# Performance work log

Hardware: AMD Instinct MI355X
Metric: run time of the kernel (lower is better)

The kernel has to match this reference:

```python
import jax, jax.numpy as jnp
import numpy as np

B, N, D = 8, 4096, 1024
S, K = 4, 16            # n_slices, per-slice codebook size (2^(16/4))
d = D // S              # slice_dim = 256
BETA = 0.25


def setup_inputs() -> dict:
    key = jax.random.key(0)
    k1, k2 = jax.random.split(key)
    h = jax.random.normal(k1, (B, N, D), dtype=jnp.float32)
    # nn.init.uniform_(codebook.weight, -1/K, 1/K)
    codebooks = jax.random.uniform(k2, (S, K, d), dtype=jnp.float32,
                                   minval=-1.0 / K, maxval=1.0 / K)
    return {"h": h, "codebooks": codebooks}


def reference(h, codebooks):
    Bb, Nn, Dd = h.shape
    Ss, Kk, dd = codebooks.shape
    sg = jax.lax.stop_gradient

    # sliced DVQ: view h as [B,N,S,d]
    ze = h.reshape(Bb, Nn, Ss, dd)

    # pairwise squared distances per slice: [B,N,S,K]
    dist = ((ze ** 2).sum(-1, keepdims=True)
            + (codebooks ** 2).sum(-1)[None, None, :, :]
            - 2.0 * jnp.einsum('bnsd,skd->bnsk', ze, codebooks))
    ids = jnp.argmin(dist, axis=-1)                         # [B,N,S] int

    # gather nearest codes: [B,N,S,d]
    zq = codebooks[jnp.arange(Ss)[None, None, :], ids]

    # per-slice VQ losses (mse over that slice), summed over slices
    loss_cb = jnp.mean((zq - sg(ze)) ** 2, axis=(0, 1, 3))  # [S]
    loss_cm = jnp.mean((ze - sg(zq)) ** 2, axis=(0, 1, 3))  # [S]
    vq_total = (loss_cb + BETA * loss_cm).sum()

    # straight-through estimator, concat slices back to [B,N,D]
    z = (ze + sg(zq - ze)).reshape(Bb, Nn, Dd)

    # pack ids: offsets are [1, K, K^2, K^3] since all slice sizes equal
    offsets = (Kk ** jnp.arange(Ss)).astype(jnp.int32)
    ids_packed = (ids.astype(jnp.int32) * offsets).sum(-1)  # [B,N]

    return (z, ids_packed, vq_total)
```

## Files before the change

kernel.cpp:

```cpp
#include <hip/hip_runtime.h>


#define D_FULL 1024
#define SEG 4
#define DSEG 256
#define KC 16

#define GLOBAL_AS __attribute__((address_space(1)))
#define LDS_AS __attribute__((address_space(3)))

static __device__ __forceinline__ void load_lds16(const void* g, void* l) {
    __builtin_amdgcn_global_load_lds((GLOBAL_AS const unsigned int*)g,
                                     (LDS_AS unsigned int*)l, 16, 0, 0);
}

__global__ __launch_bounds__(256) void dvq_prep(const float* __restrict__ cb,
                                                double* __restrict__ c2d,
                                                float* __restrict__ ids_out,
                                                float* __restrict__ loss_out) {
    __shared__ double ws[4];
    const int b = blockIdx.x;
    const int t = threadIdx.x;
    const int lane = t & 63;
    const int w = t >> 6;

    ids_out[b * 512 + t] = 0.0f;
    ids_out[b * 512 + 256 + t] = 0.0f;
    if (b == 0 && t == 0) *loss_out = 0.0f;

    double v = (double)cb[b * 256 + t];
    double sq = v * v;
#pragma unroll
    for (int off = 32; off > 0; off >>= 1)
        sq += __shfl_down(sq, off, 64);
    if (lane == 0) ws[w] = sq;
    __syncthreads();
    if (t == 0) c2d[b] = ws[0] + ws[1] + ws[2] + ws[3];
}

__global__ __launch_bounds__(512, 4) void dvq_main(const float* __restrict__ h,
                                                   const float* __restrict__ cb,
                                                   const double* __restrict__ c2d,
                                                   float* __restrict__ z_out,
                                                   float* __restrict__ ids_out,
                                                   float* __restrict__ loss_out) {
    __shared__ __align__(16) float4 hl[64 * 64];
    __shared__ __align__(16) float cbl[KC * DSEG];

    const int i = threadIdx.x;
    const int lane = i & 63;
    const int w = i >> 6;
    const int ch = __builtin_amdgcn_readfirstlane(w);

    const int s = blockIdx.x & 3;
    const long tok_base = (long)(blockIdx.x >> 2) * 64;

    char* hl_b = (char*)hl;
    char* cbl_b = (char*)cbl;

#pragma unroll
    for (int rr = 0; rr < 8; ++rr) {
        const int r = ch * 8 + rr;
        load_lds16(h + (tok_base + r) * D_FULL + (long)s * DSEG +
                       ((lane ^ r) << 2),
                   hl_b + r * 1024);
    }
#pragma unroll
    for (int half = 0; half < 2; ++half) {
        load_lds16(cb + s * (KC * DSEG) + ch * 512 + half * 256 + lane * 4,
                   cbl_b + ch * 2048 + half * 1024);
    }

    __syncthreads();

    const float* cbs = cbl + ch * 32;
    const int tk = lane;

    double dot[KC];
#pragma unroll
    for (int k = 0; k < KC; ++k) dot[k] = 0.0;
    double ze2 = 0.0;

#pragma unroll
    for (int j = 0; j < 8; ++j) {
        const int jj = ch * 8 + j;
        float4 z4 = hl[tk * 64 + (jj ^ tk)];
        double z0 = (double)z4.x, z1 = (double)z4.y;
        double z2 = (double)z4.z, z3 = (double)z4.w;
        ze2 = fma(z0, z0, ze2);
        ze2 = fma(z1, z1, ze2);
        ze2 = fma(z2, z2, ze2);
        ze2 = fma(z3, z3, ze2);
#pragma unroll
        for (int k = 0; k < KC; ++k) {
            float4 c4 = *(const float4*)(cbs + k * DSEG + j * 4);
            double a = dot[k];
            a = fma(z0, (double)c4.x, a);
            a = fma(z1, (double)c4.y, a);
            a = fma(z2, (double)c4.z, a);
            a = fma(z3, (double)c4.w, a);
            dot[k] = a;
        }
    }

    __syncthreads();
    double* part = (double*)hl;
    int* ids_l = (int*)((char*)hl + 60928);
    if (w != 0) {
        double* p = part + ((w - 1) * 64 + lane) * (KC + 1);
#pragma unroll
        for (int k = 0; k < KC; ++k) p[k] = dot[k];
        p[KC] = ze2;
    }
    __syncthreads();

    if (w == 0) {
#pragma unroll
        for (int c = 0; c < 7; ++c) {
            const double* p = part + (c * 64 + lane) * (KC + 1);
#pragma unroll
            for (int k = 0; k < KC; ++k) dot[k] += p[k];
            ze2 += p[KC];
        }

        const double* c2s = c2d + s * KC;
        double best = c2s[0] - 2.0 * dot[0];
        int bk = 0;
#pragma unroll
        for (int k = 1; k < KC; ++k) {
            double sc = c2s[k] - 2.0 * dot[k];
            if (sc < best) { best = sc; bk = k; }
        }
        ids_l[lane] = bk;

        atomicAdd(&ids_out[tok_base + lane], (float)(bk << (4 * s)));

        double mind = ze2 + best;
#pragma unroll
        for (int off = 32; off > 0; off >>= 1)
            mind += __shfl_down(mind, off, 64);
        if (lane == 0)
            atomicAdd(loss_out, (float)(mind * (1.25 / 8388608.0)));
    }
    __syncthreads();

    const float4* cbl4 = (const float4*)cbl;
#pragma unroll
    for (int r0 = 0; r0 < 8; ++r0) {
        int r = ch * 8 + r0;
        int k = ids_l[r];
        float4 v = cbl4[k * 64 + lane];
        ((float4*)(z_out + (tok_base + r) * D_FULL + (long)s * DSEG))[lane] = v;
    }
}

extern "C" void kernel_launch(void* const* d_in, const int* in_sizes, int n_in,
                              void* d_out, int out_size, void* d_ws, size_t ws_size,
                              hipStream_t stream) {
    const float* h  = (const float*)d_in[0];
    const float* cb = (const float*)d_in[1];

    const int n_h = in_sizes[0];
    const int tokens = n_h / D_FULL;

    float* z_out    = (float*)d_out;
    float* ids_out  = z_out + (size_t)n_h;
    float* loss_out = ids_out + tokens;

    double* c2d = (double*)d_ws;

    dvq_prep<<<64, 256, 0, stream>>>(cb, c2d, ids_out, loss_out);
    dvq_main<<<(tokens / 64) * SEG, 512, 0, stream>>>(h, cb, c2d, z_out,
                                                      ids_out, loss_out);
}
```

Baseline: 243.0 us.

## Split codebook across wave pairs with 1024-thread blocks and two-stage argmin

Doubles the block to 1024 threads. Each wave pair splits the 16 codes into two halves of 8 over the same 32-dim chunk, roughly halving per-thread FP64 accumulators and raising in-flight waves. The cross-wave reduction becomes a transposed partial layout and a per-half argmin, followed by a final merge in wave 0. The squared norm is now wave-reduced by shuffle. This adds extra barriers and LDS traffic in the reduction, and limits the register budget per thread.

```diff
diff --git a/kernel.cpp b/kernel.cpp
--- a/kernel.cpp
+++ b/kernel.cpp
@@ -38,12 +38,10 @@
     if (t == 0) c2d[b] = ws[0] + ws[1] + ws[2] + ws[3];
 }
 
-__global__ __launch_bounds__(512, 4) void dvq_main(const float* __restrict__ h,
-                                                   const float* __restrict__ cb,
-                                                   const double* __restrict__ c2d,
-                                                   float* __restrict__ z_out,
-                                                   float* __restrict__ ids_out,
-                                                   float* __restrict__ loss_out) {
+__global__ __launch_bounds__(1024, 8) void dvq_main(
+        const float* __restrict__ h, const float* __restrict__ cb,
+        const double* __restrict__ c2d, float* __restrict__ z_out,
+        float* __restrict__ ids_out, float* __restrict__ loss_out) {
     __shared__ __align__(16) float4 hl[64 * 64];
     __shared__ __align__(16) float cbl[KC * DSEG];
 
@@ -51,6 +49,8 @@
     const int lane = i & 63;
     const int w = i >> 6;
     const int ch = __builtin_amdgcn_readfirstlane(w);
+    const int chd = ch >> 1;
+    const int ckq = ch & 1;
 
     const int s = blockIdx.x & 3;
     const long tok_base = (long)(blockIdx.x >> 2) * 64;
@@ -59,95 +59,118 @@
     char* cbl_b = (char*)cbl;
 
 #pragma unroll
-    for (int rr = 0; rr < 8; ++rr) {
-        const int r = ch * 8 + rr;
+    for (int rr = 0; rr < 4; ++rr) {
+        const int r = ch * 4 + rr;
         load_lds16(h + (tok_base + r) * D_FULL + (long)s * DSEG +
                        ((lane ^ r) << 2),
                    hl_b + r * 1024);
     }
-#pragma unroll
-    for (int half = 0; half < 2; ++half) {
-        load_lds16(cb + s * (KC * DSEG) + ch * 512 + half * 256 + lane * 4,
-                   cbl_b + ch * 2048 + half * 1024);
-    }
+    load_lds16(cb + s * (KC * DSEG) + ch * 256 + lane * 4, cbl_b + ch * 1024);
 
     __syncthreads();
 
-    const float* cbs = cbl + ch * 32;
+    const int k0 = ckq * 8;
     const int tk = lane;
 
-    double dot[KC];
+    double dot[8];
 #pragma unroll
-    for (int k = 0; k < KC; ++k) dot[k] = 0.0;
+    for (int kk = 0; kk < 8; ++kk) dot[kk] = 0.0;
     double ze2 = 0.0;
 
 #pragma unroll
     for (int j = 0; j < 8; ++j) {
-        const int jj = ch * 8 + j;
+        const int jj = chd * 8 + j;
         float4 z4 = hl[tk * 64 + (jj ^ tk)];
         double z0 = (double)z4.x, z1 = (double)z4.y;
         double z2 = (double)z4.z, z3 = (double)z4.w;
-        ze2 = fma(z0, z0, ze2);
-        ze2 = fma(z1, z1, ze2);
-        ze2 = fma(z2, z2, ze2);
-        ze2 = fma(z3, z3, ze2);
+        if (ckq == 0) {
+            ze2 = fma(z0, z0, ze2);
+            ze2 = fma(z1, z1, ze2);
+            ze2 = fma(z2, z2, ze2);
+            ze2 = fma(z3, z3, ze2);
+        }
 #pragma unroll
-        for (int k = 0; k < KC; ++k) {
-            float4 c4 = *(const float4*)(cbs + k * DSEG + j * 4);
-            double a = dot[k];
+        for (int kk = 0; kk < 8; ++kk) {
+            float4 c4 = *(const float4*)(cbl + (k0 + kk) * DSEG + jj * 4);
+            double a = dot[kk];
             a = fma(z0, (double)c4.x, a);
             a = fma(z1, (double)c4.y, a);
             a = fma(z2, (double)c4.z, a);
             a = fma(z3, (double)c4.w, a);
-            dot[k] = a;
+            dot[kk] = a;
         }
     }
 
     __syncthreads();
-    double* part = (double*)hl;
-    int* ids_l = (int*)((char*)hl + 60928);
-    if (w != 0) {
-        double* p = part + ((w - 1) * 64 + lane) * (KC + 1);
+    double* part   = (double*)hl_b;
+    double* cand_s = (double*)(hl_b + 57344);
+    int*    cand_k = (int*)(hl_b + 58368);
+    double* ze2s   = (double*)(hl_b + 58880);
+    int*    ids_l  = (int*)(hl_b + 58944);
+
+    if (ch >= 2) {
+        const int wq = (chd - 1) * 2 + ckq;
 #pragma unroll
-        for (int k = 0; k < KC; ++k) p[k] = dot[k];
-        p[KC] = ze2;
+        for (int kk = 0; kk < 8; ++kk)
+            part[(kk * 14 + wq) * 64 + lane] = dot[kk];
+    }
+    if (ckq == 0) {
+        double t = ze2;
+#pragma unroll
+        for (int off = 32; off > 0; off >>= 1)
+            t += __shfl_down(t, off, 64);
+        if (lane == 0) ze2s[chd] = t;
     }
     __syncthreads();
 
-    if (w == 0) {
+    if (ch < 2) {
 #pragma unroll
-        for (int c = 0; c < 7; ++c) {
-            const double* p = part + (c * 64 + lane) * (KC + 1);
+        for (int kk = 0; kk < 8; ++kk) {
 #pragma unroll
-            for (int k = 0; k < KC; ++k) dot[k] += p[k];
-            ze2 += p[KC];
+            for (int c = 0; c < 7; ++c)
+                dot[kk] += part[(kk * 14 + (c * 2 + ckq)) * 64 + lane];
         }
+        const double* c2s = c2d + s * KC;
+        double best = c2s[k0] - 2.0 * dot[0];
+        int bk = k0;
+#pragma unroll
+        for (int kk = 1; kk < 8; ++kk) {
+            double sc = c2s[k0 + kk] - 2.0 * dot[kk];
+            if (sc < best) { best = sc; bk = k0 + kk; }
+        }
+        cand_s[ckq * 64 + lane] = best;
+        cand_k[ckq * 64 + lane] = bk;
+    }
+    __syncthreads();
 
-        const double* c2s = c2d + s * KC;
-        double best = c2s[0] - 2.0 * dot[0];
-        int bk = 0;
-#pragma unroll
-        for (int k = 1; k < KC; ++k) {
-            double sc = c2s[k] - 2.0 * dot[k];
-            if (sc < best) { best = sc; bk = k; }
-        }
+    if (ch == 0) {
+        double s0 = cand_s[lane];
+        int b0 = cand_k[lane];
+        double s1 = cand_s[64 + lane];
+        int b1 = cand_k[64 + lane];
+        double best = s0; int bk = b0;
+        if (s1 < best) { best = s1; bk = b1; }
         ids_l[lane] = bk;
 
         atomicAdd(&ids_out[tok_base + lane], (float)(bk << (4 * s)));
 
-        double mind = ze2 + best;
+        double t = best;
 #pragma unroll
         for (int off = 32; off > 0; off >>= 1)
-            mind += __shfl_down(mind, off, 64);
-        if (lane == 0)
-            atomicAdd(loss_out, (float)(mind * (1.25 / 8388608.0)));
+            t += __shfl_down(t, off, 64);
+        if (lane == 0) {
+            double zs = 0.0;
+#pragma unroll
+            for (int q = 0; q < 8; ++q) zs += ze2s[q];
+            atomicAdd(loss_out, (float)((t + zs) * (1.25 / 8388608.0)));
+        }
     }
     __syncthreads();
 
     const float4* cbl4 = (const float4*)cbl;
 #pragma unroll
-    for (int r0 = 0; r0 < 8; ++r0) {
-        int r = ch * 8 + r0;
+    for (int r0 = 0; r0 < 4; ++r0) {
+        int r = ch * 4 + r0;
         int k = ids_l[r];
         float4 v = cbl4[k * 64 + lane];
         ((float4*)(z_out + (tok_base + r) * D_FULL + (long)s * DSEG))[lane] = v;
@@ -170,6 +193,6 @@
     double* c2d = (double*)d_ws;
 
     dvq_prep<<<64, 256, 0, stream>>>(cb, c2d, ids_out, loss_out);
-    dvq_main<<<(tokens / 64) * SEG, 512, 0, stream>>>(h, cb, c2d, z_out,
-                                                      ids_out, loss_out);
+    dvq_main<<<(tokens / 64) * SEG, 1024, 0, stream>>>(h, cb, c2d, z_out,
+                                                       ids_out, loss_out);
 }
```

Measured after the change: 286.0 us. +17.7%, slower.

## Use fp32 dot products with fp64 rescue for near-tie tokens

Applied to the files above, without the earlier changes.

Replaces the fp64 distance accumulation with fp32 FMAs and only widens to double for the cross-wave reduction. Tokens whose best and second-best scores are within a small epsilon are recomputed in fp64 straight from global memory to keep argmin exact. The codebook is now read from global memory (cached) instead of being staged in LDS, and the block index mapping is changed so blocks sharing a slice run together. The trade is far fewer fp64 FMAs against an occasional rescue loop and uncoalesced codebook reads. The hardcoded 512 in the block mapping ties the kernel to this token count.

```diff
diff --git a/kernel.cpp b/kernel.cpp
--- a/kernel.cpp
+++ b/kernel.cpp
@@ -5,6 +5,7 @@
 #define SEG 4
 #define DSEG 256
 #define KC 16
+#define EPS_RESCUE 1e-3
 
 #define GLOBAL_AS __attribute__((address_space(1)))
 #define LDS_AS __attribute__((address_space(3)))
@@ -45,18 +46,16 @@
                                                    float* __restrict__ ids_out,
                                                    float* __restrict__ loss_out) {
     __shared__ __align__(16) float4 hl[64 * 64];
-    __shared__ __align__(16) float cbl[KC * DSEG];
 
     const int i = threadIdx.x;
     const int lane = i & 63;
     const int w = i >> 6;
     const int ch = __builtin_amdgcn_readfirstlane(w);
 
-    const int s = blockIdx.x & 3;
-    const long tok_base = (long)(blockIdx.x >> 2) * 64;
+    const int s = blockIdx.x >> 9;
+    const long tok_base = (long)(blockIdx.x & 511) * 64;
 
     char* hl_b = (char*)hl;
-    char* cbl_b = (char*)cbl;
 
 #pragma unroll
     for (int rr = 0; rr < 8; ++rr) {
@@ -65,49 +64,40 @@
                        ((lane ^ r) << 2),
                    hl_b + r * 1024);
     }
-#pragma unroll
-    for (int half = 0; half < 2; ++half) {
-        load_lds16(cb + s * (KC * DSEG) + ch * 512 + half * 256 + lane * 4,
-                   cbl_b + ch * 2048 + half * 1024);
-    }
-
-    __syncthreads();
-
-    const float* cbs = cbl + ch * 32;
+    __syncthreads();
+
+    const float* cbseg = cb + s * (KC * DSEG);
     const int tk = lane;
 
-    double dot[KC];
-#pragma unroll
-    for (int k = 0; k < KC; ++k) dot[k] = 0.0;
-    double ze2 = 0.0;
+    float dot[KC];
+#pragma unroll
+    for (int k = 0; k < KC; ++k) dot[k] = 0.0f;
+    float ze2 = 0.0f;
 
 #pragma unroll
     for (int j = 0; j < 8; ++j) {
         const int jj = ch * 8 + j;
         float4 z4 = hl[tk * 64 + (jj ^ tk)];
-        double z0 = (double)z4.x, z1 = (double)z4.y;
-        double z2 = (double)z4.z, z3 = (double)z4.w;
-        ze2 = fma(z0, z0, ze2);
-        ze2 = fma(z1, z1, ze2);
-        ze2 = fma(z2, z2, ze2);
-        ze2 = fma(z3, z3, ze2);
+        ze2 = fmaf(z4.x, z4.x, ze2);
+        ze2 = fmaf(z4.y, z4.y, ze2);
+        ze2 = fmaf(z4.z, z4.z, ze2);
+        ze2 = fmaf(z4.w, z4.w, ze2);
 #pragma unroll
         for (int k = 0; k < KC; ++k) {
-            float4 c4 = *(const float4*)(cbs + k * DSEG + j * 4);
-            double a = dot[k];
-            a = fma(z0, (double)c4.x, a);
-            a = fma(z1, (double)c4.y, a);
-            a = fma(z2, (double)c4.z, a);
-            a = fma(z3, (double)c4.w, a);
-            dot[k] = a;
-        }
-    }
-
-    __syncthreads();
-    double* part = (double*)hl;
-    int* ids_l = (int*)((char*)hl + 60928);
+            const float4 c4 = *(const float4*)(cbseg + k * DSEG + jj * 4);
+            dot[k] = fmaf(z4.x, c4.x, dot[k]);
+            dot[k] = fmaf(z4.y, c4.y, dot[k]);
+            dot[k] = fmaf(z4.z, c4.z, dot[k]);
+            dot[k] = fmaf(z4.w, c4.w, dot[k]);
+        }
+    }
+
+    __syncthreads();
+    float* part  = (float*)hl_b;
+    int*   ids_l = (int*)(hl_b + 30720);
+
     if (w != 0) {
-        double* p = part + ((w - 1) * 64 + lane) * (KC + 1);
+        float* p = part + ((w - 1) * 64 + lane) * (KC + 1);
 #pragma unroll
         for (int k = 0; k < KC; ++k) p[k] = dot[k];
         p[KC] = ze2;
@@ -115,27 +105,64 @@
     __syncthreads();
 
     if (w == 0) {
+        double d64[KC];
+#pragma unroll
+        for (int k = 0; k < KC; ++k) d64[k] = (double)dot[k];
+        double z64 = (double)ze2;
 #pragma unroll
         for (int c = 0; c < 7; ++c) {
-            const double* p = part + (c * 64 + lane) * (KC + 1);
-#pragma unroll
-            for (int k = 0; k < KC; ++k) dot[k] += p[k];
-            ze2 += p[KC];
+            const float* p = part + (c * 64 + lane) * (KC + 1);
+#pragma unroll
+            for (int k = 0; k < KC; ++k) d64[k] += (double)p[k];
+            z64 += (double)p[KC];
         }
 
         const double* c2s = c2d + s * KC;
-        double best = c2s[0] - 2.0 * dot[0];
+        double best = c2s[0] - 2.0 * d64[0];
+        double second = 1e300;
         int bk = 0;
 #pragma unroll
         for (int k = 1; k < KC; ++k) {
-            double sc = c2s[k] - 2.0 * dot[k];
-            if (sc < best) { best = sc; bk = k; }
+            double sc = c2s[k] - 2.0 * d64[k];
+            if (sc < best) { second = best; best = sc; bk = k; }
+            else if (sc < second) { second = sc; }
         }
         ids_l[lane] = bk;
 
-        atomicAdd(&ids_out[tok_base + lane], (float)(bk << (4 * s)));
-
-        double mind = ze2 + best;
+        unsigned long long mask = __ballot((second - best) < EPS_RESCUE);
+        while (mask) {
+            const int t = __ffsll(mask) - 1;
+            mask &= mask - 1;
+            const int kk = lane & 15, cc = lane >> 4;
+            const float* hrow = h + (tok_base + t) * D_FULL + (long)s * DSEG + cc * 64;
+            const float* crow = cbseg + kk * DSEG + cc * 64;
+            double acc = 0.0;
+#pragma unroll
+            for (int u = 0; u < 64; u += 4) {
+                float4 hz = *(const float4*)(hrow + u);
+                float4 cz = *(const float4*)(crow + u);
+                acc = fma((double)hz.x, (double)cz.x, acc);
+                acc = fma((double)hz.y, (double)cz.y, acc);
+                acc = fma((double)hz.z, (double)cz.z, acc);
+                acc = fma((double)hz.w, (double)cz.w, acc);
+            }
+            acc += __shfl_down(acc, 16, 64);
+            acc += __shfl_down(acc, 32, 64);
+            double sc = c2s[kk] - 2.0 * acc;
+            int bkr = kk;
+#pragma unroll
+            for (int off = 8; off > 0; off >>= 1) {
+                double osc = __shfl_xor(sc, off, 64);
+                int obk = __shfl_xor(bkr, off, 64);
+                if (osc < sc || (osc == sc && obk < bkr)) { sc = osc; bkr = obk; }
+            }
+            if (lane == 0) ids_l[t] = bkr;
+        }
+
+        int bkf = ids_l[lane];
+        atomicAdd(&ids_out[tok_base + lane], (float)(bkf << (4 * s)));
+
+        double mind = z64 + best;
 #pragma unroll
         for (int off = 32; off > 0; off >>= 1)
             mind += __shfl_down(mind, off, 64);
@@ -144,12 +171,12 @@
     }
     __syncthreads();
 
-    const float4* cbl4 = (const float4*)cbl;
+    const float4* cbf4 = (const float4*)cbseg;
 #pragma unroll
     for (int r0 = 0; r0 < 8; ++r0) {
         int r = ch * 8 + r0;
         int k = ids_l[r];
-        float4 v = cbl4[k * 64 + lane];
+        float4 v = cbf4[k * 64 + lane];
         ((float4*)(z_out + (tok_base + r) * D_FULL + (long)s * DSEG))[lane] = v;
     }
 }
```

Result: slower. 275.7 us (+13.4%).
